# Kernel optimization log

Hardware: AMD Instinct MI355X
Metric: run time of the kernel (lower is better)

The kernel has to match this reference:

```python
import jax, jax.numpy as jnp
import numpy as np
import math

N_HEAD = 8
N_FEAT = 512
D_K = N_FEAT // N_HEAD
B, T = 4, 2048


def setup_inputs() -> dict:
    key = jax.random.key(0)
    ks = jax.random.split(key, 16)
    s = 1.0 / math.sqrt(N_FEAT)
    return {
        "x": jax.random.normal(ks[0], (B, T, N_FEAT), dtype=jnp.float32),
        "pos_emb": jax.random.normal(ks[1], (1, T, N_FEAT), dtype=jnp.float32),
        "Wq": jax.random.normal(ks[2], (N_FEAT, N_FEAT), dtype=jnp.float32) * s,
        "bq": jnp.zeros((N_FEAT,), dtype=jnp.float32),
        "Wk": jax.random.normal(ks[3], (N_FEAT, N_FEAT), dtype=jnp.float32) * s,
        "bk": jnp.zeros((N_FEAT,), dtype=jnp.float32),
        "Wv": jax.random.normal(ks[4], (N_FEAT, N_FEAT), dtype=jnp.float32) * s,
        "bv": jnp.zeros((N_FEAT,), dtype=jnp.float32),
        "Wpos": jax.random.normal(ks[5], (N_FEAT, N_FEAT), dtype=jnp.float32) * s,
        "Wout": jax.random.normal(ks[6], (N_FEAT, N_FEAT), dtype=jnp.float32) * s,
        "bout": jnp.zeros((N_FEAT,), dtype=jnp.float32),
        "pos_bias_u": jax.random.normal(ks[7], (N_HEAD, D_K), dtype=jnp.float32) * 0.05,
        "pos_bias_v": jax.random.normal(ks[8], (N_HEAD, D_K), dtype=jnp.float32) * 0.05,
    }


def reference(x, pos_emb, Wq, bq, Wk, bk, Wv, bv, Wpos, Wout, bout,
              pos_bias_u, pos_bias_v):
    b, t, f = x.shape
    h, d = N_HEAD, D_K
    # QKV projections (torch Linear: y = x @ W.T + b), split into heads -> (B,H,T,d)
    q = (jnp.einsum('btf,of->bto', x, Wq) + bq).reshape(b, t, h, d).transpose(0, 2, 1, 3)
    k = (jnp.einsum('btf,of->bto', x, Wk) + bk).reshape(b, t, h, d).transpose(0, 2, 1, 3)
    v = (jnp.einsum('btf,of->bto', x, Wv) + bv).reshape(b, t, h, d).transpose(0, 2, 1, 3)
    # positional projection: (1, T_pos, F) -> (H, T_pos, d)
    tp = pos_emb.shape[1]
    p = jnp.einsum('ptf,of->pto', pos_emb, Wpos).reshape(tp, h, d).transpose(1, 0, 2)
    q_u = q + pos_bias_u[None, :, None, :]  # (B,H,T,d)
    q_v = q + pos_bias_v[None, :, None, :]
    matrix_ac = jnp.einsum('bhtd,bhsd->bhts', q_u, k)   # content-content
    matrix_bd = jnp.einsum('bhtd,hsd->bhts', q_v, p)    # content-position
    scores = (matrix_ac + matrix_bd) / math.sqrt(d)
    attn = jax.nn.softmax(scores, axis=-1)  # dropout is identity in eval mode
    out = jnp.einsum('bhts,bhsd->bhtd', attn, v)
    out = out.transpose(0, 2, 1, 3).reshape(b, t, h * d)
    return jnp.einsum('btf,of->bto', out, Wout) + bout
```

## Files before the change

kernel.cpp:

```cpp
#include <hip/hip_runtime.h>

typedef float f4 __attribute__((ext_vector_type(4)));
typedef __attribute__((ext_vector_type(8))) short bf16x8;
typedef __attribute__((ext_vector_type(4))) float f32x4;

#define T_SEQ 2048
#define NFEAT 512
#define NHEAD 8
#define DK    64
#define BATCH 4

using gptr_t = const __attribute__((address_space(1))) void*;
using lptr_t = __attribute__((address_space(3))) void*;

static __device__ __forceinline__ short f2bf(float f) {
    unsigned u = __builtin_bit_cast(unsigned, f);
    u += 0x7fff + ((u >> 16) & 1);
    return (short)(u >> 16);
}
static __device__ __forceinline__ float b2f(short s) {
    unsigned u = ((unsigned)(unsigned short)s) << 16;
    return __builtin_bit_cast(float, u);
}

__global__ __launch_bounds__(256) void cvt_kernel(
    const float* __restrict__ x, const float* __restrict__ pos,
    const float* __restrict__ Wq, const float* __restrict__ Wk, const float* __restrict__ Wv,
    const float* __restrict__ Wpos, const float* __restrict__ Wout,
    const float* __restrict__ bq, const float* __restrict__ bk, const float* __restrict__ bv,
    short* __restrict__ xb, short* __restrict__ posb, short* __restrict__ wqkv,
    short* __restrict__ wpb, short* __restrict__ wob, float* __restrict__ bqkv)
{
    const int blk = blockIdx.x;
    const float* src; short* dst; int off;
    if      (blk < 2048) { src = x;    dst = wqkv; dst = xb;          off = blk * 2048; }
    else if (blk < 2560) { src = pos;  dst = posb;                    off = (blk - 2048) * 2048; }
    else if (blk < 2688) { src = Wq;   dst = wqkv;                    off = (blk - 2560) * 2048; }
    else if (blk < 2816) { src = Wk;   dst = wqkv + 262144;           off = (blk - 2688) * 2048; }
    else if (blk < 2944) { src = Wv;   dst = wqkv + 524288;           off = (blk - 2816) * 2048; }
    else if (blk < 3072) { src = Wpos; dst = wpb;                     off = (blk - 2944) * 2048; }
    else if (blk < 3200) { src = Wout; dst = wob;                     off = (blk - 3072) * 2048; }
    else {
        int t = threadIdx.x;
        bqkv[t]        = bq[t];        bqkv[256 + t]  = bq[256 + t];
        bqkv[512 + t]  = bk[t];        bqkv[768 + t]  = bk[256 + t];
        bqkv[1024 + t] = bv[t];        bqkv[1280 + t] = bv[256 + t];
        return;
    }
    int i = off + threadIdx.x * 8;
    f4 a = *(const f4*)(src + i);
    f4 b = *(const f4*)(src + i + 4);
    bf16x8 o;
#pragma unroll
    for (int j = 0; j < 4; ++j) { o[j] = f2bf(a[j]); o[4 + j] = f2bf(b[j]); }
    *(bf16x8*)(dst + i) = o;
}

template<int OUT_BF16>
__global__ __launch_bounds__(256) void gemm_bf16(
    const short* __restrict__ A, const short* __restrict__ B,
    const float* __restrict__ bias, void* __restrict__ Cv,
    int M, int N, int K)
{
    __shared__ short As[4096];
    __shared__ short Bs[4096];
    const int tid = threadIdx.x, lane = tid & 63, wave = tid >> 6;
    const int col = lane & 15, quad = lane >> 4;
    const int wm = (wave >> 1) * 64, wn = (wave & 1) * 64;
    const int row0 = blockIdx.y * 128, col0 = blockIdx.x * 128;
    const int rl = lane & 15, kc = lane >> 4;

    const size_t Aoff = (size_t)(row0 + wave * 32 + rl) * K + kc * 8;
    const size_t Boff = (size_t)(col0 + wave * 32 + rl) * K + kc * 8;

    f32x4 acc[4][4];
#pragma unroll
    for (int i = 0; i < 4; ++i)
#pragma unroll
        for (int j = 0; j < 4; ++j) acc[i][j] = (f32x4){0.f, 0.f, 0.f, 0.f};

    for (int k0 = 0; k0 < K; k0 += 32) {
        __syncthreads();
        __builtin_amdgcn_global_load_lds((gptr_t)(A + Aoff + k0),          (lptr_t)(As + wave * 1024),       16, 0, 0);
        __builtin_amdgcn_global_load_lds((gptr_t)(A + Aoff + 16 * K + k0), (lptr_t)(As + wave * 1024 + 512), 16, 0, 0);
        __builtin_amdgcn_global_load_lds((gptr_t)(B + Boff + k0),          (lptr_t)(Bs + wave * 1024),       16, 0, 0);
        __builtin_amdgcn_global_load_lds((gptr_t)(B + Boff + 16 * K + k0), (lptr_t)(Bs + wave * 1024 + 512), 16, 0, 0);
        __syncthreads();
        bf16x8 af[4], bfr[4];
#pragma unroll
        for (int mt = 0; mt < 4; ++mt)
            af[mt] = *(const bf16x8*)&As[((wm >> 4) + mt) * 512 + quad * 128 + col * 8];
#pragma unroll
        for (int nt = 0; nt < 4; ++nt)
            bfr[nt] = *(const bf16x8*)&Bs[((wn >> 4) + nt) * 512 + quad * 128 + col * 8];
#pragma unroll
        for (int mt = 0; mt < 4; ++mt)
#pragma unroll
            for (int nt = 0; nt < 4; ++nt)
                acc[mt][nt] = __builtin_amdgcn_mfma_f32_16x16x32_bf16(af[mt], bfr[nt], acc[mt][nt], 0, 0, 0);
    }

    float bv4[4];
#pragma unroll
    for (int nt = 0; nt < 4; ++nt)
        bv4[nt] = bias ? bias[col0 + wn + nt * 16 + col] : 0.f;
#pragma unroll
    for (int mt = 0; mt < 4; ++mt)
#pragma unroll
        for (int reg = 0; reg < 4; ++reg) {
            int r = row0 + wm + mt * 16 + quad * 4 + reg;
#pragma unroll
            for (int nt = 0; nt < 4; ++nt) {
                int c = col0 + wn + nt * 16 + col;
                float v = acc[mt][nt][reg] + bv4[nt];
                if (OUT_BF16) ((short*)Cv)[(size_t)r * N + c] = f2bf(v);
                else          ((float*)Cv)[(size_t)r * N + c] = v;
            }
        }
}

__global__ __launch_bounds__(256) void kpcb_kernel(
    const short* __restrict__ qkv, const short* __restrict__ pm,
    const float* __restrict__ u, const float* __restrict__ vb,
    short* __restrict__ kp, float* __restrict__ cb)
{
    int w = blockIdx.x * 4 + (threadIdx.x >> 6);
    int lane = threadIdx.x & 63;
    int s = w & (T_SEQ - 1), bh = w >> 11, b = bh >> 3, h = bh & 7;
    float k = b2f(qkv[(size_t)(b * T_SEQ + s) * 1536 + 512 + h * DK + lane]);
    float p = b2f(pm[(size_t)s * NFEAT + h * DK + lane]);
    kp[((size_t)bh * T_SEQ + s) * DK + lane] = f2bf(k + p);
    float c = u[h * DK + lane] * k + vb[h * DK + lane] * p;
#pragma unroll
    for (int off = 1; off < 64; off <<= 1) c += __shfl_xor(c, off);
    if (lane == 0) cb[(size_t)bh * T_SEQ + s] = 0.125f * c;
}

__global__ __launch_bounds__(256) void vtr_kernel(
    const short* __restrict__ qkv, short* __restrict__ vt)
{
    __shared__ short tile[64][72];
    int tid = threadIdx.x, lr = tid >> 2, lc = (tid & 3) * 16;
    int bh = blockIdx.y, b = bh >> 3, h = bh & 7, t0 = blockIdx.x * 64;
    const short* src = qkv + (size_t)(b * T_SEQ + t0 + lr) * 1536 + 1024 + h * DK + lc;
    *(bf16x8*)&tile[lr][lc]     = *(const bf16x8*)src;
    *(bf16x8*)&tile[lr][lc + 8] = *(const bf16x8*)(src + 8);
    __syncthreads();
    short* dst = vt + (size_t)(bh * DK + lr) * T_SEQ + t0 + lc;
    bf16x8 o0, o1;
#pragma unroll
    for (int j = 0; j < 8; ++j) { o0[j] = tile[lc + j][lr]; o1[j] = tile[lc + 8 + j][lr]; }
    *(bf16x8*)dst       = o0;
    *(bf16x8*)(dst + 8) = o1;
}

__global__ __launch_bounds__(256) void attn_kernel(
    const short* __restrict__ qkv, const short* __restrict__ kp,
    const short* __restrict__ vt, const float* __restrict__ cb,
    short* __restrict__ attO)
{
    __shared__ __align__(16) short Qs[64][72], KPs[64][72], Vts[64][72], Ps[4][16][72];
    __shared__ float cs[64];
    const int tid = threadIdx.x, lane = tid & 63, wave = tid >> 6;
    const int col = lane & 15, quad = lane >> 4;
    const int bh = blockIdx.y, b = bh >> 3, h = bh & 7, t0 = blockIdx.x * 64;
    const int lr = tid >> 2, lc = (tid & 3) * 16;

    {
        const short* qp = qkv + (size_t)(b * T_SEQ + t0 + lr) * 1536 + h * DK + lc;
        *(bf16x8*)&Qs[lr][lc]     = *(const bf16x8*)qp;
        *(bf16x8*)&Qs[lr][lc + 8] = *(const bf16x8*)(qp + 8);
    }
    f32x4 Oacc[4];
    float lsum[4] = {0.f, 0.f, 0.f, 0.f};
#pragma unroll
    for (int i = 0; i < 4; ++i) Oacc[i] = (f32x4){0.f, 0.f, 0.f, 0.f};

    for (int s0 = 0; s0 < T_SEQ; s0 += 64) {
        __syncthreads();
        {
            const short* kpp = kp + ((size_t)bh * T_SEQ + s0 + lr) * DK + lc;
            *(bf16x8*)&KPs[lr][lc]     = *(const bf16x8*)kpp;
            *(bf16x8*)&KPs[lr][lc + 8] = *(const bf16x8*)(kpp + 8);
            const short* vp = vt + (size_t)(bh * DK + lr) * T_SEQ + s0 + lc;
            *(bf16x8*)&Vts[lr][lc]     = *(const bf16x8*)vp;
            *(bf16x8*)&Vts[lr][lc + 8] = *(const bf16x8*)(vp + 8);
            if (tid < 64) cs[tid] = cb[(size_t)bh * T_SEQ + s0 + tid];
        }
        __syncthreads();

        f32x4 S[4];
#pragma unroll
        for (int nt = 0; nt < 4; ++nt) S[nt] = (f32x4){0.f, 0.f, 0.f, 0.f};
#pragma unroll
        for (int kt = 0; kt < 2; ++kt) {
            bf16x8 a = *(const bf16x8*)&Qs[wave * 16 + col][kt * 32 + quad * 8];
#pragma unroll
            for (int nt = 0; nt < 4; ++nt) {
                bf16x8 bb = *(const bf16x8*)&KPs[nt * 16 + col][kt * 32 + quad * 8];
                S[nt] = __builtin_amdgcn_mfma_f32_16x16x32_bf16(a, bb, S[nt], 0, 0, 0);
            }
        }
        float c0 = cs[col], c1 = cs[16 + col], c2 = cs[32 + col], c3 = cs[48 + col];
#pragma unroll
        for (int reg = 0; reg < 4; ++reg) {
            int r = quad * 4 + reg;
            float e0 = __expf(fmaf(S[0][reg], 0.125f, c0));
            float e1 = __expf(fmaf(S[1][reg], 0.125f, c1));
            float e2 = __expf(fmaf(S[2][reg], 0.125f, c2));
            float e3 = __expf(fmaf(S[3][reg], 0.125f, c3));
            lsum[reg] += (e0 + e1) + (e2 + e3);
            Ps[wave][r][col]      = f2bf(e0);
            Ps[wave][r][16 + col] = f2bf(e1);
            Ps[wave][r][32 + col] = f2bf(e2);
            Ps[wave][r][48 + col] = f2bf(e3);
        }
        __syncthreads();
#pragma unroll
        for (int kt = 0; kt < 2; ++kt) {
            bf16x8 pa = *(const bf16x8*)&Ps[wave][col][kt * 32 + quad * 8];
#pragma unroll
            for (int dt = 0; dt < 4; ++dt) {
                bf16x8 vb = *(const bf16x8*)&Vts[dt * 16 + col][kt * 32 + quad * 8];
                Oacc[dt] = __builtin_amdgcn_mfma_f32_16x16x32_bf16(pa, vb, Oacc[dt], 0, 0, 0);
            }
        }
    }
#pragma unroll
    for (int reg = 0; reg < 4; ++reg) {
        float l = lsum[reg];
#pragma unroll
        for (int off = 1; off < 16; off <<= 1) l += __shfl_xor(l, off);
        float inv = 1.f / l;
        int t = t0 + wave * 16 + quad * 4 + reg;
        short* op = attO + (size_t)(b * T_SEQ + t) * NFEAT + h * DK;
#pragma unroll
        for (int dt = 0; dt < 4; ++dt)
            op[dt * 16 + col] = f2bf(Oacc[dt][reg] * inv);
    }
}

extern "C" void kernel_launch(void* const* d_in, const int* in_sizes, int n_in,
                              void* d_out, int out_size, void* d_ws, size_t ws_size,
                              hipStream_t stream)
{
    const float* x    = (const float*)d_in[0];
    const float* pos  = (const float*)d_in[1];
    const float* Wq   = (const float*)d_in[2];
    const float* bq   = (const float*)d_in[3];
    const float* Wk   = (const float*)d_in[4];
    const float* bk   = (const float*)d_in[5];
    const float* Wv   = (const float*)d_in[6];
    const float* bv   = (const float*)d_in[7];
    const float* Wpos = (const float*)d_in[8];
    const float* Wout = (const float*)d_in[9];
    const float* bout = (const float*)d_in[10];
    const float* pbu  = (const float*)d_in[11];
    const float* pbv  = (const float*)d_in[12];
    float* out = (float*)d_out;

    short* xb   = (short*)d_ws;
    short* posb = xb   + 4194304;
    short* wqkv = posb + 1048576;
    short* wpb  = wqkv + 786432;
    short* wob  = wpb  + 262144;
    short* QKV  = wob  + 262144;
    short* Pm   = QKV  + 12582912;
    short* KP   = Pm   + 1048576;
    short* Vt   = KP   + 4194304;
    short* AttO = Vt   + 4194304;
    float* bqkv = (float*)(AttO + 4194304);
    float* Cb   = bqkv + 1536;

    dim3 blk(256);
    cvt_kernel<<<dim3(3201), blk, 0, stream>>>(x, pos, Wq, Wk, Wv, Wpos, Wout, bq, bk, bv,
                                               xb, posb, wqkv, wpb, wob, bqkv);
    gemm_bf16<1><<<dim3(1536 / 128, 8192 / 128), blk, 0, stream>>>(xb,   wqkv, bqkv,    QKV, 8192, 1536, 512);
    gemm_bf16<1><<<dim3(512 / 128,  2048 / 128), blk, 0, stream>>>(posb, wpb,  nullptr, Pm,  2048, 512,  512);
    kpcb_kernel<<<dim3(BATCH * NHEAD * T_SEQ / 4), blk, 0, stream>>>(QKV, Pm, pbu, pbv, KP, Cb);
    vtr_kernel<<<dim3(T_SEQ / 64, BATCH * NHEAD), blk, 0, stream>>>(QKV, Vt);
    attn_kernel<<<dim3(T_SEQ / 64, BATCH * NHEAD), blk, 0, stream>>>(QKV, KP, Vt, Cb, AttO);
    gemm_bf16<0><<<dim3(512 / 128,  8192 / 128), blk, 0, stream>>>(AttO, wob, bout, out, 8192, 512, 512);
}
```

Measured before the change: 254.8 us.

## Merge QKV/pos GEMMs and K/V prep kernels, deepen GEMM K-tile, enlarge attention blocks

Merges the QKV and positional projection GEMMs into a single launch, and merges the K+P/bias-term kernel with the V transpose kernel. The GEMM K-step grows from 32 to 64, which halves the number of barriers per tile. The attention kernel now handles 128 query rows with 8 waves, so each loaded K/V tile is shared by twice as many queries. These changes aim to cut launch overhead and redundant K/V tile loads, at the cost of more LDS per block and fewer attention blocks in flight.

```diff
diff --git a/kernel.cpp b/kernel.cpp
--- a/kernel.cpp
+++ b/kernel.cpp
@@ -33,13 +33,13 @@
 {
     const int blk = blockIdx.x;
     const float* src; short* dst; int off;
-    if      (blk < 2048) { src = x;    dst = wqkv; dst = xb;          off = blk * 2048; }
-    else if (blk < 2560) { src = pos;  dst = posb;                    off = (blk - 2048) * 2048; }
-    else if (blk < 2688) { src = Wq;   dst = wqkv;                    off = (blk - 2560) * 2048; }
-    else if (blk < 2816) { src = Wk;   dst = wqkv + 262144;           off = (blk - 2688) * 2048; }
-    else if (blk < 2944) { src = Wv;   dst = wqkv + 524288;           off = (blk - 2816) * 2048; }
-    else if (blk < 3072) { src = Wpos; dst = wpb;                     off = (blk - 2944) * 2048; }
-    else if (blk < 3200) { src = Wout; dst = wob;                     off = (blk - 3072) * 2048; }
+    if      (blk < 2048) { src = x;    dst = xb;          off = blk * 2048; }
+    else if (blk < 2560) { src = pos;  dst = posb;        off = (blk - 2048) * 2048; }
+    else if (blk < 2688) { src = Wq;   dst = wqkv;        off = (blk - 2560) * 2048; }
+    else if (blk < 2816) { src = Wk;   dst = wqkv + 262144; off = (blk - 2688) * 2048; }
+    else if (blk < 2944) { src = Wv;   dst = wqkv + 524288; off = (blk - 2816) * 2048; }
+    else if (blk < 3072) { src = Wpos; dst = wpb;         off = (blk - 2944) * 2048; }
+    else if (blk < 3200) { src = Wout; dst = wob;         off = (blk - 3072) * 2048; }
     else {
         int t = threadIdx.x;
         bqkv[t]        = bq[t];        bqkv[256 + t]  = bq[256 + t];
@@ -57,21 +57,19 @@
 }
 
 template<int OUT_BF16>
-__global__ __launch_bounds__(256) void gemm_bf16(
+static __device__ __forceinline__ void gemm_tile(
+    short* As, short* Bs,
     const short* __restrict__ A, const short* __restrict__ B,
     const float* __restrict__ bias, void* __restrict__ Cv,
-    int M, int N, int K)
-{
-    __shared__ short As[4096];
-    __shared__ short Bs[4096];
+    int N, int K, int row0, int col0)
+{
     const int tid = threadIdx.x, lane = tid & 63, wave = tid >> 6;
     const int col = lane & 15, quad = lane >> 4;
     const int wm = (wave >> 1) * 64, wn = (wave & 1) * 64;
-    const int row0 = blockIdx.y * 128, col0 = blockIdx.x * 128;
-    const int rl = lane & 15, kc = lane >> 4;
-
-    const size_t Aoff = (size_t)(row0 + wave * 32 + rl) * K + kc * 8;
-    const size_t Boff = (size_t)(col0 + wave * 32 + rl) * K + kc * 8;
+    const int rl = lane & 15;
+
+    const short* Abase = A + (size_t)(row0 + wave * 32 + rl) * K + (lane >> 4) * 8;
+    const short* Bbase = B + (size_t)(col0 + wave * 32 + rl) * K + (lane >> 4) * 8;
 
     f32x4 acc[4][4];
 #pragma unroll
@@ -79,25 +77,33 @@
 #pragma unroll
         for (int j = 0; j < 4; ++j) acc[i][j] = (f32x4){0.f, 0.f, 0.f, 0.f};
 
-    for (int k0 = 0; k0 < K; k0 += 32) {
-        __syncthreads();
-        __builtin_amdgcn_global_load_lds((gptr_t)(A + Aoff + k0),          (lptr_t)(As + wave * 1024),       16, 0, 0);
-        __builtin_amdgcn_global_load_lds((gptr_t)(A + Aoff + 16 * K + k0), (lptr_t)(As + wave * 1024 + 512), 16, 0, 0);
-        __builtin_amdgcn_global_load_lds((gptr_t)(B + Boff + k0),          (lptr_t)(Bs + wave * 1024),       16, 0, 0);
-        __builtin_amdgcn_global_load_lds((gptr_t)(B + Boff + 16 * K + k0), (lptr_t)(Bs + wave * 1024 + 512), 16, 0, 0);
-        __syncthreads();
-        bf16x8 af[4], bfr[4];
-#pragma unroll
-        for (int mt = 0; mt < 4; ++mt)
-            af[mt] = *(const bf16x8*)&As[((wm >> 4) + mt) * 512 + quad * 128 + col * 8];
-#pragma unroll
-        for (int nt = 0; nt < 4; ++nt)
-            bfr[nt] = *(const bf16x8*)&Bs[((wn >> 4) + nt) * 512 + quad * 128 + col * 8];
-#pragma unroll
-        for (int mt = 0; mt < 4; ++mt)
+    for (int k0 = 0; k0 < K; k0 += 64) {
+        __syncthreads();
+#pragma unroll
+        for (int c = 0; c < 2; ++c)
+#pragma unroll
+            for (int hf = 0; hf < 2; ++hf) {
+                __builtin_amdgcn_global_load_lds((gptr_t)(Abase + (size_t)(16 * c) * K + k0 + hf * 32),
+                                                 (lptr_t)(As + wave * 2048 + c * 1024 + hf * 512), 16, 0, 0);
+                __builtin_amdgcn_global_load_lds((gptr_t)(Bbase + (size_t)(16 * c) * K + k0 + hf * 32),
+                                                 (lptr_t)(Bs + wave * 2048 + c * 1024 + hf * 512), 16, 0, 0);
+            }
+        __syncthreads();
+#pragma unroll
+        for (int kt = 0; kt < 2; ++kt) {
+            bf16x8 af[4], bfr[4];
+#pragma unroll
+            for (int mt = 0; mt < 4; ++mt)
+                af[mt] = *(const bf16x8*)&As[((wm >> 4) + mt) * 1024 + (kt * 4 + quad) * 128 + col * 8];
 #pragma unroll
             for (int nt = 0; nt < 4; ++nt)
-                acc[mt][nt] = __builtin_amdgcn_mfma_f32_16x16x32_bf16(af[mt], bfr[nt], acc[mt][nt], 0, 0, 0);
+                bfr[nt] = *(const bf16x8*)&Bs[((wn >> 4) + nt) * 1024 + (kt * 4 + quad) * 128 + col * 8];
+#pragma unroll
+            for (int mt = 0; mt < 4; ++mt)
+#pragma unroll
+                for (int nt = 0; nt < 4; ++nt)
+                    acc[mt][nt] = __builtin_amdgcn_mfma_f32_16x16x32_bf16(af[mt], bfr[nt], acc[mt][nt], 0, 0, 0);
+        }
     }
 
     float bv4[4];
@@ -119,58 +125,94 @@
         }
 }
 
-__global__ __launch_bounds__(256) void kpcb_kernel(
+__global__ __launch_bounds__(256) void gemm_qkv_pos(
+    const short* __restrict__ xb, const short* __restrict__ wqkv,
+    const float* __restrict__ bqkv, short* __restrict__ QKV,
+    const short* __restrict__ posb, const short* __restrict__ wpb,
+    short* __restrict__ Pm)
+{
+    __shared__ short As[8192], Bs[8192];
+    const int bid = blockIdx.x;
+    if (bid < 768) {
+        gemm_tile<1>(As, Bs, xb, wqkv, bqkv, QKV, 1536, 512, (bid / 12) * 128, (bid % 12) * 128);
+    } else {
+        const int t = bid - 768;
+        gemm_tile<1>(As, Bs, posb, wpb, nullptr, Pm, 512, 512, (t / 4) * 128, (t % 4) * 128);
+    }
+}
+
+__global__ __launch_bounds__(256) void gemm_out_kernel(
+    const short* __restrict__ A, const short* __restrict__ B,
+    const float* __restrict__ bias, float* __restrict__ C)
+{
+    __shared__ short As[8192], Bs[8192];
+    gemm_tile<0>(As, Bs, A, B, bias, C, 512, 512, blockIdx.y * 128, blockIdx.x * 128);
+}
+
+__global__ __launch_bounds__(256) void kvprep_kernel(
     const short* __restrict__ qkv, const short* __restrict__ pm,
     const float* __restrict__ u, const float* __restrict__ vb,
-    short* __restrict__ kp, float* __restrict__ cb)
-{
-    int w = blockIdx.x * 4 + (threadIdx.x >> 6);
-    int lane = threadIdx.x & 63;
-    int s = w & (T_SEQ - 1), bh = w >> 11, b = bh >> 3, h = bh & 7;
-    float k = b2f(qkv[(size_t)(b * T_SEQ + s) * 1536 + 512 + h * DK + lane]);
-    float p = b2f(pm[(size_t)s * NFEAT + h * DK + lane]);
-    kp[((size_t)bh * T_SEQ + s) * DK + lane] = f2bf(k + p);
-    float c = u[h * DK + lane] * k + vb[h * DK + lane] * p;
-#pragma unroll
-    for (int off = 1; off < 64; off <<= 1) c += __shfl_xor(c, off);
-    if (lane == 0) cb[(size_t)bh * T_SEQ + s] = 0.125f * c;
-}
-
-__global__ __launch_bounds__(256) void vtr_kernel(
-    const short* __restrict__ qkv, short* __restrict__ vt)
+    short* __restrict__ kp, short* __restrict__ vt, float* __restrict__ cb)
 {
     __shared__ short tile[64][72];
-    int tid = threadIdx.x, lr = tid >> 2, lc = (tid & 3) * 16;
-    int bh = blockIdx.y, b = bh >> 3, h = bh & 7, t0 = blockIdx.x * 64;
-    const short* src = qkv + (size_t)(b * T_SEQ + t0 + lr) * 1536 + 1024 + h * DK + lc;
-    *(bf16x8*)&tile[lr][lc]     = *(const bf16x8*)src;
-    *(bf16x8*)&tile[lr][lc + 8] = *(const bf16x8*)(src + 8);
+    const int tid = threadIdx.x, lr = tid >> 2, lc = (tid & 3) * 16;
+    const int bh = blockIdx.y, b = bh >> 3, h = bh & 7, s0 = blockIdx.x * 64;
+
+    const short* kptr = qkv + (size_t)(b * T_SEQ + s0 + lr) * 1536 + 512 + h * DK + lc;
+    const short* pptr = pm + (size_t)(s0 + lr) * NFEAT + h * DK + lc;
+    const short* vptr = qkv + (size_t)(b * T_SEQ + s0 + lr) * 1536 + 1024 + h * DK + lc;
+    bf16x8 k0_ = *(const bf16x8*)kptr,       k1_ = *(const bf16x8*)(kptr + 8);
+    bf16x8 p0_ = *(const bf16x8*)pptr,       p1_ = *(const bf16x8*)(pptr + 8);
+    bf16x8 v0_ = *(const bf16x8*)vptr,       v1_ = *(const bf16x8*)(vptr + 8);
+
+    float c = 0.f;
+    bf16x8 o0, o1;
+#pragma unroll
+    for (int j = 0; j < 8; ++j) {
+        float kf = b2f(k0_[j]), pf = b2f(p0_[j]);
+        o0[j] = f2bf(kf + pf);
+        c += u[h * DK + lc + j] * kf + vb[h * DK + lc + j] * pf;
+        float kf1 = b2f(k1_[j]), pf1 = b2f(p1_[j]);
+        o1[j] = f2bf(kf1 + pf1);
+        c += u[h * DK + lc + 8 + j] * kf1 + vb[h * DK + lc + 8 + j] * pf1;
+    }
+    short* kpd = kp + ((size_t)bh * T_SEQ + s0 + lr) * DK + lc;
+    *(bf16x8*)kpd       = o0;
+    *(bf16x8*)(kpd + 8) = o1;
+    c += __shfl_xor(c, 1);
+    c += __shfl_xor(c, 2);
+    if ((tid & 3) == 0) cb[(size_t)bh * T_SEQ + s0 + lr] = 0.125f * c;
+
+    *(bf16x8*)&tile[lr][lc]     = v0_;
+    *(bf16x8*)&tile[lr][lc + 8] = v1_;
     __syncthreads();
-    short* dst = vt + (size_t)(bh * DK + lr) * T_SEQ + t0 + lc;
-    bf16x8 o0, o1;
-#pragma unroll
-    for (int j = 0; j < 8; ++j) { o0[j] = tile[lc + j][lr]; o1[j] = tile[lc + 8 + j][lr]; }
-    *(bf16x8*)dst       = o0;
-    *(bf16x8*)(dst + 8) = o1;
-}
-
-__global__ __launch_bounds__(256) void attn_kernel(
+    short* dst = vt + (size_t)(bh * DK + lr) * T_SEQ + s0 + lc;
+    bf16x8 t0_, t1_;
+#pragma unroll
+    for (int j = 0; j < 8; ++j) { t0_[j] = tile[lc + j][lr]; t1_[j] = tile[lc + 8 + j][lr]; }
+    *(bf16x8*)dst       = t0_;
+    *(bf16x8*)(dst + 8) = t1_;
+}
+
+__global__ __launch_bounds__(512) void attn_kernel(
     const short* __restrict__ qkv, const short* __restrict__ kp,
     const short* __restrict__ vt, const float* __restrict__ cb,
     short* __restrict__ attO)
 {
-    __shared__ __align__(16) short Qs[64][72], KPs[64][72], Vts[64][72], Ps[4][16][72];
+    __shared__ __align__(16) short Qs[128][72], KPs[64][72], Vts[64][72], Ps[8][16][72];
     __shared__ float cs[64];
     const int tid = threadIdx.x, lane = tid & 63, wave = tid >> 6;
     const int col = lane & 15, quad = lane >> 4;
-    const int bh = blockIdx.y, b = bh >> 3, h = bh & 7, t0 = blockIdx.x * 64;
-    const int lr = tid >> 2, lc = (tid & 3) * 16;
+    const int bh = blockIdx.y, b = bh >> 3, h = bh & 7, t0 = blockIdx.x * 128;
 
     {
+        const int lr = tid >> 2, lc = (tid & 3) * 16;
         const short* qp = qkv + (size_t)(b * T_SEQ + t0 + lr) * 1536 + h * DK + lc;
         *(bf16x8*)&Qs[lr][lc]     = *(const bf16x8*)qp;
         *(bf16x8*)&Qs[lr][lc + 8] = *(const bf16x8*)(qp + 8);
     }
+    const int lr8 = tid >> 3, lc8 = (tid & 7) * 8;
+
     f32x4 Oacc[4];
     float lsum[4] = {0.f, 0.f, 0.f, 0.f};
 #pragma unroll
@@ -178,15 +220,9 @@
 
     for (int s0 = 0; s0 < T_SEQ; s0 += 64) {
         __syncthreads();
-        {
-            const short* kpp = kp + ((size_t)bh * T_SEQ + s0 + lr) * DK + lc;
-            *(bf16x8*)&KPs[lr][lc]     = *(const bf16x8*)kpp;
-            *(bf16x8*)&KPs[lr][lc + 8] = *(const bf16x8*)(kpp + 8);
-            const short* vp = vt + (size_t)(bh * DK + lr) * T_SEQ + s0 + lc;
-            *(bf16x8*)&Vts[lr][lc]     = *(const bf16x8*)vp;
-            *(bf16x8*)&Vts[lr][lc + 8] = *(const bf16x8*)(vp + 8);
-            if (tid < 64) cs[tid] = cb[(size_t)bh * T_SEQ + s0 + tid];
-        }
+        *(bf16x8*)&KPs[lr8][lc8] = *(const bf16x8*)(kp + ((size_t)bh * T_SEQ + s0 + lr8) * DK + lc8);
+        *(bf16x8*)&Vts[lr8][lc8] = *(const bf16x8*)(vt + (size_t)(bh * DK + lr8) * T_SEQ + s0 + lc8);
+        if (tid < 64) cs[tid] = cb[(size_t)bh * T_SEQ + s0 + tid];
         __syncthreads();
 
         f32x4 S[4];
@@ -272,13 +308,10 @@
     float* bqkv = (float*)(AttO + 4194304);
     float* Cb   = bqkv + 1536;
 
-    dim3 blk(256);
-    cvt_kernel<<<dim3(3201), blk, 0, stream>>>(x, pos, Wq, Wk, Wv, Wpos, Wout, bq, bk, bv,
-                                               xb, posb, wqkv, wpb, wob, bqkv);
-    gemm_bf16<1><<<dim3(1536 / 128, 8192 / 128), blk, 0, stream>>>(xb,   wqkv, bqkv,    QKV, 8192, 1536, 512);
-    gemm_bf16<1><<<dim3(512 / 128,  2048 / 128), blk, 0, stream>>>(posb, wpb,  nullptr, Pm,  2048, 512,  512);
-    kpcb_kernel<<<dim3(BATCH * NHEAD * T_SEQ / 4), blk, 0, stream>>>(QKV, Pm, pbu, pbv, KP, Cb);
-    vtr_kernel<<<dim3(T_SEQ / 64, BATCH * NHEAD), blk, 0, stream>>>(QKV, Vt);
-    attn_kernel<<<dim3(T_SEQ / 64, BATCH * NHEAD), blk, 0, stream>>>(QKV, KP, Vt, Cb, AttO);
-    gemm_bf16<0><<<dim3(512 / 128,  8192 / 128), blk, 0, stream>>>(AttO, wob, bout, out, 8192, 512, 512);
-}
+    cvt_kernel<<<dim3(3201), dim3(256), 0, stream>>>(x, pos, Wq, Wk, Wv, Wpos, Wout, bq, bk, bv,
+                                                     xb, posb, wqkv, wpb, wob, bqkv);
+    gemm_qkv_pos<<<dim3(832), dim3(256), 0, stream>>>(xb, wqkv, bqkv, QKV, posb, wpb, Pm);
+    kvprep_kernel<<<dim3(T_SEQ / 64, BATCH * NHEAD), dim3(256), 0, stream>>>(QKV, Pm, pbu, pbv, KP, Vt, Cb);
+    attn_kernel<<<dim3(T_SEQ / 128, BATCH * NHEAD), dim3(512), 0, stream>>>(QKV, KP, Vt, Cb, AttO);
+    gemm_out_kernel<<<dim3(512 / 128, 8192 / 128), dim3(256), 0, stream>>>(AttO, wob, bout, out);
+}
```

Result: faster. 236.0 us (-7.4%).
